# Kernel optimization log

Hardware: AMD Instinct MI355X
Metric: run time of the kernel (lower is better)

Reference implementation:

```python
import jax, jax.numpy as jnp
import numpy as np

N_NODES = 50000
N_EDGES = 800000
N_GRAPHS = 128
IN_C, HID_C, OUT_C = 128, 256, 128


def setup_inputs() -> dict:
    key = jax.random.key(0)
    ks = jax.random.split(key, 10)
    x = jax.random.normal(ks[0], (N_NODES, IN_C), dtype=jnp.float32)
    edge_index = jax.random.randint(ks[1], (2, N_EDGES), 0, N_NODES, dtype=jnp.int32)
    batch = jnp.sort(jax.random.randint(ks[2], (N_NODES,), 0, N_GRAPHS, dtype=jnp.int32))
    def glorot(k, fan_in, fan_out):
        lim = (6.0 / (fan_in + fan_out)) ** 0.5
        return jax.random.uniform(k, (fan_in, fan_out), jnp.float32, -lim, lim)
    W1 = glorot(ks[3], IN_C, HID_C)
    b1 = jnp.zeros((HID_C,), jnp.float32)
    W2 = glorot(ks[4], HID_C, HID_C)
    b2 = jnp.zeros((HID_C,), jnp.float32)
    Wfc = glorot(ks[5], HID_C, OUT_C)
    bfc = jnp.zeros((OUT_C,), jnp.float32)
    return {"x": x, "edge_index": edge_index, "batch": batch,
            "W1": W1, "b1": b1, "W2": W2, "b2": b2, "Wfc": Wfc, "bfc": bfc}


def _gcn_conv(x, src, dst, W, b, n_nodes):
    # PyG GCNConv: h = x @ W; out[dst] += norm * h[src]; out += b
    h = x @ W  # [N, F_out]
    ones = jnp.ones(src.shape, dtype=h.dtype)
    deg = jax.ops.segment_sum(ones, dst, num_segments=n_nodes)  # in-degree incl self loops
    dinv = jnp.where(deg > 0, jax.lax.rsqrt(deg), 0.0)
    norm = dinv[src] * dinv[dst]                    # [E]
    msg = h[src] * norm[:, None]                    # gather + scale, [E, F_out]
    out = jax.ops.segment_sum(msg, dst, num_segments=n_nodes)  # scatter-add
    return out + b


def reference(x, edge_index, batch, W1, b1, W2, b2, Wfc, bfc):
    n = x.shape[0]
    loops = jnp.arange(n, dtype=edge_index.dtype)
    src = jnp.concatenate([edge_index[0], loops])   # add self loops (GCNConv default)
    dst = jnp.concatenate([edge_index[1], loops])
    h = jax.nn.relu(_gcn_conv(x, src, dst, W1, b1, n))
    h = jax.nn.relu(_gcn_conv(h, src, dst, W2, b2, n))
    # global_mean_pool keyed by batch index
    sums = jax.ops.segment_sum(h, batch, num_segments=N_GRAPHS)          # [G, HID]
    cnts = jax.ops.segment_sum(jnp.ones((n,), h.dtype), batch, num_segments=N_GRAPHS)
    pooled = sums / jnp.maximum(cnts, 1.0)[:, None]
    return pooled @ Wfc + bfc
```

## Files before the change

### kernel.cpp

```cpp
#include <hip/hip_runtime.h>
#include <type_traits>

#define HID 256
#define INC 128
#define OUTC 128

typedef __attribute__((ext_vector_type(8))) short short8;
typedef __attribute__((ext_vector_type(4))) float floatx4;

__device__ __forceinline__ unsigned short f2bf(float f) {
    unsigned int u = __float_as_uint(f);
    unsigned int r = (u + 0x7FFFu + ((u >> 16) & 1u)) >> 16;
    return (unsigned short)r;
}

__device__ __forceinline__ void bfacc2(float* a, uint u, float nr) {
    a[0] = fmaf(nr, __uint_as_float(u << 16), a[0]);
    a[1] = fmaf(nr, __uint_as_float(u & 0xFFFF0000u), a[1]);
}

__global__ void k_hist(const int* __restrict__ dst, int* __restrict__ cnt, int e) {
    int i = blockIdx.x * blockDim.x + threadIdx.x;
    if (i < e) atomicAdd(&cnt[dst[i]], 1);
}

__global__ __launch_bounds__(256) void k_scan_local(const int* __restrict__ cnt,
                                                    int* __restrict__ ex, int* __restrict__ blk_sum,
                                                    float* __restrict__ dinv, int n) {
    __shared__ int s[256];
    const int t = threadIdx.x;
    const int i = blockIdx.x * 256 + t;
    const int v = (i < n) ? cnt[i] : 0;
    if (i < n) dinv[i] = rsqrtf((float)v + 1.0f);
    s[t] = v;
    __syncthreads();
    for (int off = 1; off < 256; off <<= 1) {
        int add = (t >= off) ? s[t - off] : 0;
        __syncthreads();
        s[t] += add;
        __syncthreads();
    }
    if (i < n) ex[i] = s[t] - v;
    if (t == 255) blk_sum[blockIdx.x] = s[255];
}

__global__ __launch_bounds__(256) void k_scan_add(int* __restrict__ row_ptr,
                                                  const int* __restrict__ blk_sum,
                                                  int* __restrict__ cnt, int n, int e) {
    __shared__ int s[256];
    const int t = threadIdx.x;
    const int b = blockIdx.x;
    s[t] = (t < b) ? blk_sum[t] : 0;
    __syncthreads();
    for (int off = 128; off > 0; off >>= 1) {
        if (t < off) s[t] += s[t + off];
        __syncthreads();
    }
    const int offset = s[0];
    const int i = b * 256 + t;
    if (i < n) { row_ptr[i] += offset; cnt[i] = 0; }
    if (i == 0) row_ptr[n] = e;
}

__global__ void k_fill(const int* __restrict__ src, const int* __restrict__ dst,
                       const int* __restrict__ row_ptr, int* __restrict__ cursor,
                       int2* __restrict__ csr, const float* __restrict__ dinv, int e) {
    int i = blockIdx.x * blockDim.x + threadIdx.x;
    if (i < e) {
        const int d = dst[i];
        const int s = src[i];
        const int pos = row_ptr[d] + atomicAdd(&cursor[d], 1);
        csr[pos] = make_int2(s, __float_as_int(dinv[s] * dinv[d]));
    }
}

__global__ void k_conv(const float* __restrict__ x, unsigned short* __restrict__ xb,
                       const float* __restrict__ W1, unsigned short* __restrict__ Wt1,
                       const float* __restrict__ W2, unsigned short* __restrict__ Wt2,
                       int* __restrict__ cnt, float* __restrict__ pooled,
                       int nx4, int n) {
    const int id = blockIdx.x * 256 + threadIdx.x;
    if (id < n) cnt[id] = 0;
    if (id < 128 * HID) pooled[id] = 0.0f;
    if (id < nx4) {
        const float4 v = *(const float4*)(x + (size_t)id * 4);
        uint2 o;
        o.x = (unsigned)f2bf(v.x) | ((unsigned)f2bf(v.y) << 16);
        o.y = (unsigned)f2bf(v.z) | ((unsigned)f2bf(v.w) << 16);
        *(uint2*)(xb + (size_t)id * 4) = o;
        return;
    }
    const int id2 = id - nx4;
    if (id2 < INC * HID) {
        const int nn = id2 / INC;
        const int kk = id2 - nn * INC;
        Wt1[id2] = f2bf(W1[kk * HID + nn]);
        return;
    }
    const int id3 = id2 - INC * HID;
    if (id3 < HID * HID) {
        const int nn = id3 / HID;
        const int kk = id3 - nn * HID;
        Wt2[id3] = f2bf(W2[kk * HID + nn]);
    }
}

template <int CH>
__global__ __launch_bounds__(256) void k_agg(const unsigned short* __restrict__ h,
                                             const int* __restrict__ row_ptr,
                                             const int2* __restrict__ csr,
                                             const float* __restrict__ dinv,
                                             unsigned short* __restrict__ out,
                                             int v0, int vend) {
    constexpr int CPL = CH / 32;
    using VT = std::conditional_t<CPL == 4, uint2, uint4>;
    const int v = v0 + ((blockIdx.x * 256 + threadIdx.x) >> 5);
    const int l = threadIdx.x & 31;
    if (v >= vend) return;
    const float dv = dinv[v];
    const unsigned short* hl = h + l * CPL;

    float acc[CPL];
    {
        const VT u = *(const VT*)(hl + (size_t)v * CH);
        const float s2 = dv * dv;
        if constexpr (CPL == 4) {
            const uint2 w = (uint2)u;
            acc[0] = s2 * __uint_as_float(w.x << 16);
            acc[1] = s2 * __uint_as_float(w.x & 0xFFFF0000u);
            acc[2] = s2 * __uint_as_float(w.y << 16);
            acc[3] = s2 * __uint_as_float(w.y & 0xFFFF0000u);
        } else {
            const uint4 w = (uint4)u;
            acc[0] = s2 * __uint_as_float(w.x << 16);
            acc[1] = s2 * __uint_as_float(w.x & 0xFFFF0000u);
            acc[2] = s2 * __uint_as_float(w.y << 16);
            acc[3] = s2 * __uint_as_float(w.y & 0xFFFF0000u);
            acc[4] = s2 * __uint_as_float(w.z << 16);
            acc[5] = s2 * __uint_as_float(w.z & 0xFFFF0000u);
            acc[6] = s2 * __uint_as_float(w.w << 16);
            acc[7] = s2 * __uint_as_float(w.w & 0xFFFF0000u);
        }
    }

    const int beg = row_ptr[v];
    const int end = row_ptr[v + 1];
    int i = beg;
    for (; i + 8 <= end; i += 8) {
        int2 p[8];
#pragma unroll
        for (int k = 0; k < 8; ++k) p[k] = csr[i + k];
        VT r[8];
#pragma unroll
        for (int k = 0; k < 8; ++k) r[k] = *(const VT*)(hl + (size_t)p[k].x * CH);
#pragma unroll
        for (int k = 0; k < 8; ++k) {
            const float nr = __int_as_float(p[k].y);
            if constexpr (CPL == 4) {
                const uint2 w = (uint2)r[k];
                bfacc2(acc, w.x, nr); bfacc2(acc + 2, w.y, nr);
            } else {
                const uint4 w = (uint4)r[k];
                bfacc2(acc, w.x, nr); bfacc2(acc + 2, w.y, nr);
                bfacc2(acc + 4, w.z, nr); bfacc2(acc + 6, w.w, nr);
            }
        }
    }
    for (; i < end; ++i) {
        const int2 p0 = csr[i];
        const float nr = __int_as_float(p0.y);
        const VT r0 = *(const VT*)(hl + (size_t)p0.x * CH);
        if constexpr (CPL == 4) {
            const uint2 w = (uint2)r0;
            bfacc2(acc, w.x, nr); bfacc2(acc + 2, w.y, nr);
        } else {
            const uint4 w = (uint4)r0;
            bfacc2(acc, w.x, nr); bfacc2(acc + 2, w.y, nr);
            bfacc2(acc + 4, w.z, nr); bfacc2(acc + 6, w.w, nr);
        }
    }

    if constexpr (CPL == 4) {
        uint2 o;
        o.x = (unsigned)f2bf(acc[0]) | ((unsigned)f2bf(acc[1]) << 16);
        o.y = (unsigned)f2bf(acc[2]) | ((unsigned)f2bf(acc[3]) << 16);
        *(uint2*)(out + (size_t)v * CH + l * 4) = o;
    } else {
        uint4 o;
        o.x = (unsigned)f2bf(acc[0]) | ((unsigned)f2bf(acc[1]) << 16);
        o.y = (unsigned)f2bf(acc[2]) | ((unsigned)f2bf(acc[3]) << 16);
        o.z = (unsigned)f2bf(acc[4]) | ((unsigned)f2bf(acc[5]) << 16);
        o.w = (unsigned)f2bf(acc[6]) | ((unsigned)f2bf(acc[7]) << 16);
        *(uint4*)(out + (size_t)v * CH + l * 8) = o;
    }
}

template <int K, bool RELU, bool POOL, typename OT>
__global__ __launch_bounds__(256, 2) void k_gemm_p(const unsigned short* __restrict__ A,
                                                   const unsigned short* __restrict__ Wt,
                                                   const float* __restrict__ bias,
                                                   OT* __restrict__ out,
                                                   const int* __restrict__ batch,
                                                   float* __restrict__ pooled_sum,
                                                   int M, int ntiles) {
    const int t = threadIdx.x;
    const int wv = t >> 6;
    const int lane = t & 63;
    const int m16 = lane & 15;
    const int quad = lane >> 4;
    const int nbase = wv * 64 + m16;

    short8 Bf[4][K / 32];
    {
        const unsigned short* bp = Wt + (size_t)nbase * K + quad * 8;
#pragma unroll
        for (int nt = 0; nt < 4; ++nt)
#pragma unroll
            for (int ks = 0; ks < K / 32; ++ks)
                Bf[nt][ks] = *(const short8*)(bp + nt * 16 * K + ks * 32);
    }
    const float bb0 = bias[nbase + 0];
    const float bb1 = bias[nbase + 16];
    const float bb2 = bias[nbase + 32];
    const float bb3 = bias[nbase + 48];
    const short8 z8 = {0, 0, 0, 0, 0, 0, 0, 0};

    for (int tile = blockIdx.x; tile < ntiles; tile += gridDim.x) {
        const int row0 = tile * 32;
        floatx4 acc[2][4];
#pragma unroll
        for (int h2 = 0; h2 < 2; ++h2)
#pragma unroll
            for (int j = 0; j < 4; ++j) acc[h2][j] = (floatx4){0.f, 0.f, 0.f, 0.f};

        const unsigned short* ar0 = A + (size_t)(row0 + m16) * K + quad * 8;
        if (row0 + 32 <= M) {
#pragma unroll
            for (int ks = 0; ks < K / 32; ++ks) {
                const short8 a0 = *(const short8*)(ar0 + ks * 32);
                const short8 a1 = *(const short8*)(ar0 + 16 * K + ks * 32);
                acc[0][0] = __builtin_amdgcn_mfma_f32_16x16x32_bf16(a0, Bf[0][ks], acc[0][0], 0, 0, 0);
                acc[0][1] = __builtin_amdgcn_mfma_f32_16x16x32_bf16(a0, Bf[1][ks], acc[0][1], 0, 0, 0);
                acc[0][2] = __builtin_amdgcn_mfma_f32_16x16x32_bf16(a0, Bf[2][ks], acc[0][2], 0, 0, 0);
                acc[0][3] = __builtin_amdgcn_mfma_f32_16x16x32_bf16(a0, Bf[3][ks], acc[0][3], 0, 0, 0);
                acc[1][0] = __builtin_amdgcn_mfma_f32_16x16x32_bf16(a1, Bf[0][ks], acc[1][0], 0, 0, 0);
                acc[1][1] = __builtin_amdgcn_mfma_f32_16x16x32_bf16(a1, Bf[1][ks], acc[1][1], 0, 0, 0);
                acc[1][2] = __builtin_amdgcn_mfma_f32_16x16x32_bf16(a1, Bf[2][ks], acc[1][2], 0, 0, 0);
                acc[1][3] = __builtin_amdgcn_mfma_f32_16x16x32_bf16(a1, Bf[3][ks], acc[1][3], 0, 0, 0);
            }
        } else {
            const bool r0ok = (row0 + m16) < M;
            const bool r1ok = (row0 + 16 + m16) < M;
#pragma unroll
            for (int ks = 0; ks < K / 32; ++ks) {
                short8 a0 = z8, a1 = z8;
                if (r0ok) a0 = *(const short8*)(ar0 + ks * 32);
                if (r1ok) a1 = *(const short8*)(ar0 + 16 * K + ks * 32);
                acc[0][0] = __builtin_amdgcn_mfma_f32_16x16x32_bf16(a0, Bf[0][ks], acc[0][0], 0, 0, 0);
                acc[0][1] = __builtin_amdgcn_mfma_f32_16x16x32_bf16(a0, Bf[1][ks], acc[0][1], 0, 0, 0);
                acc[0][2] = __builtin_amdgcn_mfma_f32_16x16x32_bf16(a0, Bf[2][ks], acc[0][2], 0, 0, 0);
                acc[0][3] = __builtin_amdgcn_mfma_f32_16x16x32_bf16(a0, Bf[3][ks], acc[0][3], 0, 0, 0);
                acc[1][0] = __builtin_amdgcn_mfma_f32_16x16x32_bf16(a1, Bf[0][ks], acc[1][0], 0, 0, 0);
                acc[1][1] = __builtin_amdgcn_mfma_f32_16x16x32_bf16(a1, Bf[1][ks], acc[1][1], 0, 0, 0);
                acc[1][2] = __builtin_amdgcn_mfma_f32_16x16x32_bf16(a1, Bf[2][ks], acc[1][2], 0, 0, 0);
                acc[1][3] = __builtin_amdgcn_mfma_f32_16x16x32_bf16(a1, Bf[3][ks], acc[1][3], 0, 0, 0);
            }
        }

        if constexpr (POOL) {
            float ps0 = 0.f, ps1 = 0.f, ps2 = 0.f, ps3 = 0.f;
            int gcur = -1;
#pragma unroll
            for (int h2 = 0; h2 < 2; ++h2) {
#pragma unroll
                for (int j = 0; j < 4; ++j) {
                    const int row = row0 + h2 * 16 + quad * 4 + j;
                    const int g = (row < M) ? batch[row] : -1;
                    if (g < 0) continue;
                    if (g != gcur) {
                        if (gcur >= 0) {
                            float* pp = pooled_sum + gcur * HID + nbase;
                            atomicAdd(pp + 0, ps0);
                            atomicAdd(pp + 16, ps1);
                            atomicAdd(pp + 32, ps2);
                            atomicAdd(pp + 48, ps3);
                        }
                        ps0 = ps1 = ps2 = ps3 = 0.f;
                        gcur = g;
                    }
                    ps0 += fmaxf(acc[h2][0][j] + bb0, 0.f);
                    ps1 += fmaxf(acc[h2][1][j] + bb1, 0.f);
                    ps2 += fmaxf(acc[h2][2][j] + bb2, 0.f);
                    ps3 += fmaxf(acc[h2][3][j] + bb3, 0.f);
                }
            }
            if (gcur >= 0) {
                float* pp = pooled_sum + gcur * HID + nbase;
                atomicAdd(pp + 0, ps0);
                atomicAdd(pp + 16, ps1);
                atomicAdd(pp + 32, ps2);
                atomicAdd(pp + 48, ps3);
            }
        } else {
#pragma unroll
            for (int h2 = 0; h2 < 2; ++h2) {
#pragma unroll
                for (int j = 0; j < 4; ++j) {
                    const int row = row0 + h2 * 16 + quad * 4 + j;
                    if (row >= M) continue;
                    float v0 = acc[h2][0][j] + bb0;
                    float v1 = acc[h2][1][j] + bb1;
                    float v2 = acc[h2][2][j] + bb2;
                    float v3 = acc[h2][3][j] + bb3;
                    if constexpr (RELU) {
                        v0 = fmaxf(v0, 0.f); v1 = fmaxf(v1, 0.f);
                        v2 = fmaxf(v2, 0.f); v3 = fmaxf(v3, 0.f);
                    }
                    out[(size_t)row * HID + nbase + 0]  = (OT)f2bf(v0);
                    out[(size_t)row * HID + nbase + 16] = (OT)f2bf(v1);
                    out[(size_t)row * HID + nbase + 32] = (OT)f2bf(v2);
                    out[(size_t)row * HID + nbase + 48] = (OT)f2bf(v3);
                }
            }
        }
    }
}

__global__ void k_fc(const float* __restrict__ pooled_sum, const int* __restrict__ batch,
                     const float* __restrict__ W, const float* __restrict__ b,
                     float* __restrict__ out, int n) {
    const int g = blockIdx.x;
    const int c = threadIdx.x;
    int a = 0, hi = n;
    while (a < hi) { int m = (a + hi) >> 1; if (batch[m] < g) a = m + 1; else hi = m; }
    const int start = a;
    hi = n;
    while (a < hi) { int m = (a + hi) >> 1; if (batch[m] < g + 1) a = m + 1; else hi = m; }
    const float cnt = (float)(a - start);

    float acc = 0.0f;
    const float* p = pooled_sum + g * HID;
    for (int k = 0; k < HID; ++k) acc += p[k] * W[k * OUTC + c];
    out[g * OUTC + c] = acc / fmaxf(cnt, 1.0f) + b[c];
}

extern "C" void kernel_launch(void* const* d_in, const int* in_sizes, int n_in,
                              void* d_out, int out_size, void* d_ws, size_t ws_size,
                              hipStream_t stream) {
    const float* x   = (const float*)d_in[0];
    const int*   ei  = (const int*)d_in[1];
    const int*   bat = (const int*)d_in[2];
    const float* W1  = (const float*)d_in[3];
    const float* b1  = (const float*)d_in[4];
    const float* W2  = (const float*)d_in[5];
    const float* b2  = (const float*)d_in[6];
    const float* Wfc = (const float*)d_in[7];
    const float* bfc = (const float*)d_in[8];
    float* out = (float*)d_out;

    const int n = in_sizes[2];
    const int e = in_sizes[1] / 2;
    const int* src = ei;
    const int* dst = ei + e;
    const int nb = (n + 255) / 256;

    size_t off = 0;
    auto alloc = [&](size_t bytes) {
        char* p = (char*)d_ws + off;
        off += (bytes + 255) & ~(size_t)255;
        return p;
    };
    int*   cnt     = (int*)alloc((size_t)n * 4);
    int*   row_ptr = (int*)alloc((size_t)(n + 1) * 4);
    int*   blk_sum = (int*)alloc(512 * 4);
    int2*  csr     = (int2*)alloc((size_t)e * 8);
    float* dinv    = (float*)alloc((size_t)n * 4);
    unsigned short* Wt1 = (unsigned short*)alloc((size_t)INC * HID * 2);
    unsigned short* Wt2 = (unsigned short*)alloc((size_t)HID * HID * 2);
    unsigned short* R1  = (unsigned short*)alloc((size_t)n * HID * 2);
    unsigned short* R2  = (unsigned short*)alloc((size_t)n * INC * 2);
    unsigned short* R3  = (unsigned short*)alloc((size_t)n * HID * 2);
    float* pooled = (float*)alloc((size_t)128 * HID * 4);

    const int TB = 256;
    const int nx4 = n * INC / 4;

    k_conv<<<(nx4 + INC * HID + HID * HID + TB - 1) / TB, TB, 0, stream>>>(
        x, R1, W1, Wt1, W2, Wt2, cnt, pooled, nx4, n);

    k_hist<<<(e + TB - 1) / TB, TB, 0, stream>>>(dst, cnt, e);
    k_scan_local<<<nb, TB, 0, stream>>>(cnt, row_ptr, blk_sum, dinv, n);
    k_scan_add<<<nb, TB, 0, stream>>>(row_ptr, blk_sum, cnt, n, e);
    k_fill<<<(e + TB - 1) / TB, TB, 0, stream>>>(src, dst, row_ptr, cnt, csr, dinv, e);

    const int ntiles = (n + 31) / 32;
    const int GEMM_GRID = 512;

    const int half = (n + 1) / 2;
    const int ab1 = (half + 7) / 8;
    const int ab2 = (n - half + 7) / 8;

    k_agg<INC><<<ab1, TB, 0, stream>>>(R1, row_ptr, csr, dinv, R2, 0, half);
    k_agg<INC><<<ab2, TB, 0, stream>>>(R1, row_ptr, csr, dinv, R2, half, n);
    k_gemm_p<INC, true, false, unsigned short><<<GEMM_GRID, TB, 0, stream>>>(
        R2, Wt1, b1, R3, nullptr, nullptr, n, ntiles);

    k_agg<HID><<<ab1, TB, 0, stream>>>(R3, row_ptr, csr, dinv, R1, 0, half);
    k_agg<HID><<<ab2, TB, 0, stream>>>(R3, row_ptr, csr, dinv, R1, half, n);
    k_gemm_p<HID, true, true, float><<<GEMM_GRID, TB, 0, stream>>>(
        R1, Wt2, b2, (float*)nullptr, bat, pooled, n, ntiles);

    k_fc<<<128, 128, 0, stream>>>(pooled, bat, Wfc, bfc, out, n);
}
```

Before: 355.2 us.

## Fuse preprocessing into cooperative kernel, un-split aggregation, one-tile-per-block GEMM

Merges the conversion, histogram, and two scan kernels into a single cooperative kernel that uses grid-wide syncs between phases, which removes several launches. The aggregation kernels now run as one launch per layer instead of two halves. The GEMM drops its persistent tile loop and launches one block per 32-row tile, so each block reloads the weight fragments into registers. Grid syncs and extra per-block weight loads add cost, and the 1024-block cooperative launch relies on enough occupancy to be accepted.

```diff
diff --git a/kernel.cpp b/kernel.cpp
--- a/kernel.cpp
+++ b/kernel.cpp
@@ -1,5 +1,8 @@
 #include <hip/hip_runtime.h>
+#include <hip/hip_cooperative_groups.h>
 #include <type_traits>
+
+namespace cg = cooperative_groups;
 
 #define HID 256
 #define INC 128
@@ -19,47 +22,81 @@
     a[1] = fmaf(nr, __uint_as_float(u & 0xFFFF0000u), a[1]);
 }
 
-__global__ void k_hist(const int* __restrict__ dst, int* __restrict__ cnt, int e) {
-    int i = blockIdx.x * blockDim.x + threadIdx.x;
-    if (i < e) atomicAdd(&cnt[dst[i]], 1);
-}
-
-__global__ __launch_bounds__(256) void k_scan_local(const int* __restrict__ cnt,
-                                                    int* __restrict__ ex, int* __restrict__ blk_sum,
-                                                    float* __restrict__ dinv, int n) {
+__global__ __launch_bounds__(256) void k_csr_coop(
+    const float* __restrict__ x, unsigned short* __restrict__ xb,
+    const float* __restrict__ W1, unsigned short* __restrict__ Wt1,
+    const float* __restrict__ W2, unsigned short* __restrict__ Wt2,
+    int* __restrict__ cnt, float* __restrict__ pooled,
+    const int* __restrict__ dst,
+    int* __restrict__ row_ptr, int* __restrict__ blk_sum,
+    float* __restrict__ dinv,
+    int nx4, int n, int e, int nb) {
+    cg::grid_group grid = cg::this_grid();
     __shared__ int s[256];
     const int t = threadIdx.x;
-    const int i = blockIdx.x * 256 + t;
-    const int v = (i < n) ? cnt[i] : 0;
-    if (i < n) dinv[i] = rsqrtf((float)v + 1.0f);
-    s[t] = v;
-    __syncthreads();
-    for (int off = 1; off < 256; off <<= 1) {
-        int add = (t >= off) ? s[t - off] : 0;
+    const int gsz = gridDim.x * 256;
+    const int gid0 = blockIdx.x * 256 + t;
+
+    const int TOT = nx4 + INC * HID + HID * HID;
+    for (int id = gid0; id < TOT; id += gsz) {
+        if (id < n) cnt[id] = 0;
+        if (id < 128 * HID) pooled[id] = 0.0f;
+        if (id < nx4) {
+            const float4 v = *(const float4*)(x + (size_t)id * 4);
+            uint2 o;
+            o.x = (unsigned)f2bf(v.x) | ((unsigned)f2bf(v.y) << 16);
+            o.y = (unsigned)f2bf(v.z) | ((unsigned)f2bf(v.w) << 16);
+            *(uint2*)(xb + (size_t)id * 4) = o;
+        } else {
+            const int id2 = id - nx4;
+            if (id2 < INC * HID) {
+                const int nn = id2 / INC;
+                const int kk = id2 - nn * INC;
+                Wt1[id2] = f2bf(W1[kk * HID + nn]);
+            } else {
+                const int id3 = id2 - INC * HID;
+                if (id3 < HID * HID) {
+                    const int nn = id3 / HID;
+                    const int kk = id3 - nn * HID;
+                    Wt2[id3] = f2bf(W2[kk * HID + nn]);
+                }
+            }
+        }
+    }
+    grid.sync();
+
+    for (int i = gid0; i < e; i += gsz) atomicAdd(&cnt[dst[i]], 1);
+    grid.sync();
+
+    if (blockIdx.x < nb) {
+        const int i = blockIdx.x * 256 + t;
+        const int v = (i < n) ? cnt[i] : 0;
+        if (i < n) dinv[i] = rsqrtf((float)v + 1.0f);
+        s[t] = v;
         __syncthreads();
-        s[t] += add;
+        for (int off = 1; off < 256; off <<= 1) {
+            int add = (t >= off) ? s[t - off] : 0;
+            __syncthreads();
+            s[t] += add;
+            __syncthreads();
+        }
+        if (i < n) row_ptr[i] = s[t] - v;
+        if (t == 255) blk_sum[blockIdx.x] = s[255];
+    }
+    grid.sync();
+
+    if (blockIdx.x < nb) {
+        s[t] = (t < blockIdx.x) ? blk_sum[t] : 0;
         __syncthreads();
-    }
-    if (i < n) ex[i] = s[t] - v;
-    if (t == 255) blk_sum[blockIdx.x] = s[255];
-}
-
-__global__ __launch_bounds__(256) void k_scan_add(int* __restrict__ row_ptr,
-                                                  const int* __restrict__ blk_sum,
-                                                  int* __restrict__ cnt, int n, int e) {
-    __shared__ int s[256];
-    const int t = threadIdx.x;
-    const int b = blockIdx.x;
-    s[t] = (t < b) ? blk_sum[t] : 0;
-    __syncthreads();
-    for (int off = 128; off > 0; off >>= 1) {
-        if (t < off) s[t] += s[t + off];
-        __syncthreads();
-    }
-    const int offset = s[0];
-    const int i = b * 256 + t;
-    if (i < n) { row_ptr[i] += offset; cnt[i] = 0; }
-    if (i == 0) row_ptr[n] = e;
+        for (int off = 128; off > 0; off >>= 1) {
+            if (t < off) s[t] += s[t + off];
+            __syncthreads();
+        }
+        const int offset = s[0];
+        const int i = blockIdx.x * 256 + t;
+        if (i < n) { row_ptr[i] += offset; cnt[i] = 0; }
+        if (i == 0) row_ptr[n] = e;
+    }
 }
 
 __global__ void k_fill(const int* __restrict__ src, const int* __restrict__ dst,
@@ -74,49 +111,17 @@
     }
 }
 
-__global__ void k_conv(const float* __restrict__ x, unsigned short* __restrict__ xb,
-                       const float* __restrict__ W1, unsigned short* __restrict__ Wt1,
-                       const float* __restrict__ W2, unsigned short* __restrict__ Wt2,
-                       int* __restrict__ cnt, float* __restrict__ pooled,
-                       int nx4, int n) {
-    const int id = blockIdx.x * 256 + threadIdx.x;
-    if (id < n) cnt[id] = 0;
-    if (id < 128 * HID) pooled[id] = 0.0f;
-    if (id < nx4) {
-        const float4 v = *(const float4*)(x + (size_t)id * 4);
-        uint2 o;
-        o.x = (unsigned)f2bf(v.x) | ((unsigned)f2bf(v.y) << 16);
-        o.y = (unsigned)f2bf(v.z) | ((unsigned)f2bf(v.w) << 16);
-        *(uint2*)(xb + (size_t)id * 4) = o;
-        return;
-    }
-    const int id2 = id - nx4;
-    if (id2 < INC * HID) {
-        const int nn = id2 / INC;
-        const int kk = id2 - nn * INC;
-        Wt1[id2] = f2bf(W1[kk * HID + nn]);
-        return;
-    }
-    const int id3 = id2 - INC * HID;
-    if (id3 < HID * HID) {
-        const int nn = id3 / HID;
-        const int kk = id3 - nn * HID;
-        Wt2[id3] = f2bf(W2[kk * HID + nn]);
-    }
-}
-
 template <int CH>
 __global__ __launch_bounds__(256) void k_agg(const unsigned short* __restrict__ h,
                                              const int* __restrict__ row_ptr,
                                              const int2* __restrict__ csr,
                                              const float* __restrict__ dinv,
-                                             unsigned short* __restrict__ out,
-                                             int v0, int vend) {
+                                             unsigned short* __restrict__ out, int n) {
     constexpr int CPL = CH / 32;
     using VT = std::conditional_t<CPL == 4, uint2, uint4>;
-    const int v = v0 + ((blockIdx.x * 256 + threadIdx.x) >> 5);
+    const int v = (blockIdx.x * 256 + threadIdx.x) >> 5;
     const int l = threadIdx.x & 31;
-    if (v >= vend) return;
+    if (v >= n) return;
     const float dv = dinv[v];
     const unsigned short* hl = h + l * CPL;
 
@@ -196,19 +201,19 @@
 }
 
 template <int K, bool RELU, bool POOL, typename OT>
-__global__ __launch_bounds__(256, 2) void k_gemm_p(const unsigned short* __restrict__ A,
-                                                   const unsigned short* __restrict__ Wt,
-                                                   const float* __restrict__ bias,
-                                                   OT* __restrict__ out,
-                                                   const int* __restrict__ batch,
-                                                   float* __restrict__ pooled_sum,
-                                                   int M, int ntiles) {
+__global__ __launch_bounds__(256, 2) void k_gemm(const unsigned short* __restrict__ A,
+                                                 const unsigned short* __restrict__ Wt,
+                                                 const float* __restrict__ bias,
+                                                 OT* __restrict__ out,
+                                                 const int* __restrict__ batch,
+                                                 float* __restrict__ pooled_sum, int M) {
     const int t = threadIdx.x;
     const int wv = t >> 6;
     const int lane = t & 63;
     const int m16 = lane & 15;
     const int quad = lane >> 4;
     const int nbase = wv * 64 + m16;
+    const int row0 = blockIdx.x * 32;
 
     short8 Bf[4][K / 32];
     {
@@ -225,102 +230,99 @@
     const float bb3 = bias[nbase + 48];
     const short8 z8 = {0, 0, 0, 0, 0, 0, 0, 0};
 
-    for (int tile = blockIdx.x; tile < ntiles; tile += gridDim.x) {
-        const int row0 = tile * 32;
-        floatx4 acc[2][4];
-#pragma unroll
-        for (int h2 = 0; h2 < 2; ++h2)
-#pragma unroll
-            for (int j = 0; j < 4; ++j) acc[h2][j] = (floatx4){0.f, 0.f, 0.f, 0.f};
-
-        const unsigned short* ar0 = A + (size_t)(row0 + m16) * K + quad * 8;
-        if (row0 + 32 <= M) {
-#pragma unroll
-            for (int ks = 0; ks < K / 32; ++ks) {
-                const short8 a0 = *(const short8*)(ar0 + ks * 32);
-                const short8 a1 = *(const short8*)(ar0 + 16 * K + ks * 32);
-                acc[0][0] = __builtin_amdgcn_mfma_f32_16x16x32_bf16(a0, Bf[0][ks], acc[0][0], 0, 0, 0);
-                acc[0][1] = __builtin_amdgcn_mfma_f32_16x16x32_bf16(a0, Bf[1][ks], acc[0][1], 0, 0, 0);
-                acc[0][2] = __builtin_amdgcn_mfma_f32_16x16x32_bf16(a0, Bf[2][ks], acc[0][2], 0, 0, 0);
-                acc[0][3] = __builtin_amdgcn_mfma_f32_16x16x32_bf16(a0, Bf[3][ks], acc[0][3], 0, 0, 0);
-                acc[1][0] = __builtin_amdgcn_mfma_f32_16x16x32_bf16(a1, Bf[0][ks], acc[1][0], 0, 0, 0);
-                acc[1][1] = __builtin_amdgcn_mfma_f32_16x16x32_bf16(a1, Bf[1][ks], acc[1][1], 0, 0, 0);
-                acc[1][2] = __builtin_amdgcn_mfma_f32_16x16x32_bf16(a1, Bf[2][ks], acc[1][2], 0, 0, 0);
-                acc[1][3] = __builtin_amdgcn_mfma_f32_16x16x32_bf16(a1, Bf[3][ks], acc[1][3], 0, 0, 0);
+    floatx4 acc[2][4];
+#pragma unroll
+    for (int h2 = 0; h2 < 2; ++h2)
+#pragma unroll
+        for (int j = 0; j < 4; ++j) acc[h2][j] = (floatx4){0.f, 0.f, 0.f, 0.f};
+
+    const unsigned short* ar0 = A + (size_t)(row0 + m16) * K + quad * 8;
+    if (row0 + 32 <= M) {
+#pragma unroll
+        for (int ks = 0; ks < K / 32; ++ks) {
+            const short8 a0 = *(const short8*)(ar0 + ks * 32);
+            const short8 a1 = *(const short8*)(ar0 + 16 * K + ks * 32);
+            acc[0][0] = __builtin_amdgcn_mfma_f32_16x16x32_bf16(a0, Bf[0][ks], acc[0][0], 0, 0, 0);
+            acc[0][1] = __builtin_amdgcn_mfma_f32_16x16x32_bf16(a0, Bf[1][ks], acc[0][1], 0, 0, 0);
+            acc[0][2] = __builtin_amdgcn_mfma_f32_16x16x32_bf16(a0, Bf[2][ks], acc[0][2], 0, 0, 0);
+            acc[0][3] = __builtin_amdgcn_mfma_f32_16x16x32_bf16(a0, Bf[3][ks], acc[0][3], 0, 0, 0);
+            acc[1][0] = __builtin_amdgcn_mfma_f32_16x16x32_bf16(a1, Bf[0][ks], acc[1][0], 0, 0, 0);
+            acc[1][1] = __builtin_amdgcn_mfma_f32_16x16x32_bf16(a1, Bf[1][ks], acc[1][1], 0, 0, 0);
+            acc[1][2] = __builtin_amdgcn_mfma_f32_16x16x32_bf16(a1, Bf[2][ks], acc[1][2], 0, 0, 0);
+            acc[1][3] = __builtin_amdgcn_mfma_f32_16x16x32_bf16(a1, Bf[3][ks], acc[1][3], 0, 0, 0);
+        }
+    } else {
+        const bool r0ok = (row0 + m16) < M;
+        const bool r1ok = (row0 + 16 + m16) < M;
+#pragma unroll
+        for (int ks = 0; ks < K / 32; ++ks) {
+            short8 a0 = z8, a1 = z8;
+            if (r0ok) a0 = *(const short8*)(ar0 + ks * 32);
+            if (r1ok) a1 = *(const short8*)(ar0 + 16 * K + ks * 32);
+            acc[0][0] = __builtin_amdgcn_mfma_f32_16x16x32_bf16(a0, Bf[0][ks], acc[0][0], 0, 0, 0);
+            acc[0][1] = __builtin_amdgcn_mfma_f32_16x16x32_bf16(a0, Bf[1][ks], acc[0][1], 0, 0, 0);
+            acc[0][2] = __builtin_amdgcn_mfma_f32_16x16x32_bf16(a0, Bf[2][ks], acc[0][2], 0, 0, 0);
+            acc[0][3] = __builtin_amdgcn_mfma_f32_16x16x32_bf16(a0, Bf[3][ks], acc[0][3], 0, 0, 0);
+            acc[1][0] = __builtin_amdgcn_mfma_f32_16x16x32_bf16(a1, Bf[0][ks], acc[1][0], 0, 0, 0);
+            acc[1][1] = __builtin_amdgcn_mfma_f32_16x16x32_bf16(a1, Bf[1][ks], acc[1][1], 0, 0, 0);
+            acc[1][2] = __builtin_amdgcn_mfma_f32_16x16x32_bf16(a1, Bf[2][ks], acc[1][2], 0, 0, 0);
+            acc[1][3] = __builtin_amdgcn_mfma_f32_16x16x32_bf16(a1, Bf[3][ks], acc[1][3], 0, 0, 0);
+        }
+    }
+
+    if constexpr (POOL) {
+        float ps0 = 0.f, ps1 = 0.f, ps2 = 0.f, ps3 = 0.f;
+        int gcur = -1;
+#pragma unroll
+        for (int h2 = 0; h2 < 2; ++h2) {
+#pragma unroll
+            for (int j = 0; j < 4; ++j) {
+                const int row = row0 + h2 * 16 + quad * 4 + j;
+                const int g = (row < M) ? batch[row] : -1;
+                if (g < 0) continue;
+                if (g != gcur) {
+                    if (gcur >= 0) {
+                        float* pp = pooled_sum + gcur * HID + nbase;
+                        atomicAdd(pp + 0, ps0);
+                        atomicAdd(pp + 16, ps1);
+                        atomicAdd(pp + 32, ps2);
+                        atomicAdd(pp + 48, ps3);
+                    }
+                    ps0 = ps1 = ps2 = ps3 = 0.f;
+                    gcur = g;
+                }
+                ps0 += fmaxf(acc[h2][0][j] + bb0, 0.f);
+                ps1 += fmaxf(acc[h2][1][j] + bb1, 0.f);
+                ps2 += fmaxf(acc[h2][2][j] + bb2, 0.f);
+                ps3 += fmaxf(acc[h2][3][j] + bb3, 0.f);
             }
-        } else {
-            const bool r0ok = (row0 + m16) < M;
-            const bool r1ok = (row0 + 16 + m16) < M;
-#pragma unroll
-            for (int ks = 0; ks < K / 32; ++ks) {
-                short8 a0 = z8, a1 = z8;
-                if (r0ok) a0 = *(const short8*)(ar0 + ks * 32);
-                if (r1ok) a1 = *(const short8*)(ar0 + 16 * K + ks * 32);
-                acc[0][0] = __builtin_amdgcn_mfma_f32_16x16x32_bf16(a0, Bf[0][ks], acc[0][0], 0, 0, 0);
-                acc[0][1] = __builtin_amdgcn_mfma_f32_16x16x32_bf16(a0, Bf[1][ks], acc[0][1], 0, 0, 0);
-                acc[0][2] = __builtin_amdgcn_mfma_f32_16x16x32_bf16(a0, Bf[2][ks], acc[0][2], 0, 0, 0);
-                acc[0][3] = __builtin_amdgcn_mfma_f32_16x16x32_bf16(a0, Bf[3][ks], acc[0][3], 0, 0, 0);
-                acc[1][0] = __builtin_amdgcn_mfma_f32_16x16x32_bf16(a1, Bf[0][ks], acc[1][0], 0, 0, 0);
-                acc[1][1] = __builtin_amdgcn_mfma_f32_16x16x32_bf16(a1, Bf[1][ks], acc[1][1], 0, 0, 0);
-                acc[1][2] = __builtin_amdgcn_mfma_f32_16x16x32_bf16(a1, Bf[2][ks], acc[1][2], 0, 0, 0);
-                acc[1][3] = __builtin_amdgcn_mfma_f32_16x16x32_bf16(a1, Bf[3][ks], acc[1][3], 0, 0, 0);
-            }
-        }
-
-        if constexpr (POOL) {
-            float ps0 = 0.f, ps1 = 0.f, ps2 = 0.f, ps3 = 0.f;
-            int gcur = -1;
-#pragma unroll
-            for (int h2 = 0; h2 < 2; ++h2) {
-#pragma unroll
-                for (int j = 0; j < 4; ++j) {
-                    const int row = row0 + h2 * 16 + quad * 4 + j;
-                    const int g = (row < M) ? batch[row] : -1;
-                    if (g < 0) continue;
-                    if (g != gcur) {
-                        if (gcur >= 0) {
-                            float* pp = pooled_sum + gcur * HID + nbase;
-                            atomicAdd(pp + 0, ps0);
-                            atomicAdd(pp + 16, ps1);
-                            atomicAdd(pp + 32, ps2);
-                            atomicAdd(pp + 48, ps3);
-                        }
-                        ps0 = ps1 = ps2 = ps3 = 0.f;
-                        gcur = g;
-                    }
-                    ps0 += fmaxf(acc[h2][0][j] + bb0, 0.f);
-                    ps1 += fmaxf(acc[h2][1][j] + bb1, 0.f);
-                    ps2 += fmaxf(acc[h2][2][j] + bb2, 0.f);
-                    ps3 += fmaxf(acc[h2][3][j] + bb3, 0.f);
+        }
+        if (gcur >= 0) {
+            float* pp = pooled_sum + gcur * HID + nbase;
+            atomicAdd(pp + 0, ps0);
+            atomicAdd(pp + 16, ps1);
+            atomicAdd(pp + 32, ps2);
+            atomicAdd(pp + 48, ps3);
+        }
+    } else {
+#pragma unroll
+        for (int h2 = 0; h2 < 2; ++h2) {
+#pragma unroll
+            for (int j = 0; j < 4; ++j) {
+                const int row = row0 + h2 * 16 + quad * 4 + j;
+                if (row >= M) continue;
+                float v0 = acc[h2][0][j] + bb0;
+                float v1 = acc[h2][1][j] + bb1;
+                float v2 = acc[h2][2][j] + bb2;
+                float v3 = acc[h2][3][j] + bb3;
+                if constexpr (RELU) {
+                    v0 = fmaxf(v0, 0.f); v1 = fmaxf(v1, 0.f);
+                    v2 = fmaxf(v2, 0.f); v3 = fmaxf(v3, 0.f);
                 }
-            }
-            if (gcur >= 0) {
-                float* pp = pooled_sum + gcur * HID + nbase;
-                atomicAdd(pp + 0, ps0);
-                atomicAdd(pp + 16, ps1);
-                atomicAdd(pp + 32, ps2);
-                atomicAdd(pp + 48, ps3);
-            }
-        } else {
-#pragma unroll
-            for (int h2 = 0; h2 < 2; ++h2) {
-#pragma unroll
-                for (int j = 0; j < 4; ++j) {
-                    const int row = row0 + h2 * 16 + quad * 4 + j;
-                    if (row >= M) continue;
-                    float v0 = acc[h2][0][j] + bb0;
-                    float v1 = acc[h2][1][j] + bb1;
-                    float v2 = acc[h2][2][j] + bb2;
-                    float v3 = acc[h2][3][j] + bb3;
-                    if constexpr (RELU) {
-                        v0 = fmaxf(v0, 0.f); v1 = fmaxf(v1, 0.f);
-                        v2 = fmaxf(v2, 0.f); v3 = fmaxf(v3, 0.f);
-                    }
-                    out[(size_t)row * HID + nbase + 0]  = (OT)f2bf(v0);
-                    out[(size_t)row * HID + nbase + 16] = (OT)f2bf(v1);
-                    out[(size_t)row * HID + nbase + 32] = (OT)f2bf(v2);
-                    out[(size_t)row * HID + nbase + 48] = (OT)f2bf(v3);
-                }
+                out[(size_t)row * HID + nbase + 0]  = (OT)f2bf(v0);
+                out[(size_t)row * HID + nbase + 16] = (OT)f2bf(v1);
+                out[(size_t)row * HID + nbase + 32] = (OT)f2bf(v2);
+                out[(size_t)row * HID + nbase + 48] = (OT)f2bf(v3);
             }
         }
     }
@@ -383,32 +385,33 @@
     float* pooled = (float*)alloc((size_t)128 * HID * 4);
 
     const int TB = 256;
-    const int nx4 = n * INC / 4;
-
-    k_conv<<<(nx4 + INC * HID + HID * HID + TB - 1) / TB, TB, 0, stream>>>(
-        x, R1, W1, Wt1, W2, Wt2, cnt, pooled, nx4, n);
-
-    k_hist<<<(e + TB - 1) / TB, TB, 0, stream>>>(dst, cnt, e);
-    k_scan_local<<<nb, TB, 0, stream>>>(cnt, row_ptr, blk_sum, dinv, n);
-    k_scan_add<<<nb, TB, 0, stream>>>(row_ptr, blk_sum, cnt, n, e);
+    int nx4 = n * INC / 4;
+    int n_ = n, e_ = e, nb_ = nb;
+
+    {
+        unsigned short* xb = R1;
+        void* args[] = {
+            (void*)&x, (void*)&xb, (void*)&W1, (void*)&Wt1, (void*)&W2, (void*)&Wt2,
+            (void*)&cnt, (void*)&pooled, (void*)&dst,
+            (void*)&row_ptr, (void*)&blk_sum, (void*)&dinv,
+            (void*)&nx4, (void*)&n_, (void*)&e_, (void*)&nb_
+        };
+        hipLaunchCooperativeKernel((const void*)k_csr_coop, dim3(1024), dim3(TB),
+                                   args, 0, stream);
+    }
+
     k_fill<<<(e + TB - 1) / TB, TB, 0, stream>>>(src, dst, row_ptr, cnt, csr, dinv, e);
 
     const int ntiles = (n + 31) / 32;
-    const int GEMM_GRID = 512;
-
-    const int half = (n + 1) / 2;
-    const int ab1 = (half + 7) / 8;
-    const int ab2 = (n - half + 7) / 8;
-
-    k_agg<INC><<<ab1, TB, 0, stream>>>(R1, row_ptr, csr, dinv, R2, 0, half);
-    k_agg<INC><<<ab2, TB, 0, stream>>>(R1, row_ptr, csr, dinv, R2, half, n);
-    k_gemm_p<INC, true, false, unsigned short><<<GEMM_GRID, TB, 0, stream>>>(
-        R2, Wt1, b1, R3, nullptr, nullptr, n, ntiles);
-
-    k_agg<HID><<<ab1, TB, 0, stream>>>(R3, row_ptr, csr, dinv, R1, 0, half);
-    k_agg<HID><<<ab2, TB, 0, stream>>>(R3, row_ptr, csr, dinv, R1, half, n);
-    k_gemm_p<HID, true, true, float><<<GEMM_GRID, TB, 0, stream>>>(
-        R1, Wt2, b2, (float*)nullptr, bat, pooled, n, ntiles);
+    const int agg_blocks = (n + 7) / 8;
+
+    k_agg<INC><<<agg_blocks, TB, 0, stream>>>(R1, row_ptr, csr, dinv, R2, n);
+    k_gemm<INC, true, false, unsigned short><<<ntiles, TB, 0, stream>>>(
+        R2, Wt1, b1, R3, nullptr, nullptr, n);
+
+    k_agg<HID><<<agg_blocks, TB, 0, stream>>>(R3, row_ptr, csr, dinv, R1, n);
+    k_gemm<HID, true, true, float><<<ntiles, TB, 0, stream>>>(
+        R1, Wt2, b2, (float*)nullptr, bat, pooled, n);
 
     k_fc<<<128, 128, 0, stream>>>(pooled, bat, Wfc, bfc, out, n);
 }
```

Measured after the change: 665.7 us. 1.87x slower.
